# Kernel tuning notes

Measured on AMD Instinct MI355X. Metric: run time of the kernel, lower is better.

The kernel has to match this reference:

```python
import jax, jax.numpy as jnp
import numpy as np

B = 16384
D = 64            # bottom_mlp_layers[-1] = embedding_dim
DENSE = 512
HIST = 50         # history length per row
C_CAMP = 1000     # num_collisions for campaign table (sqrt(1e6))
C_FEAT = 316      # num_collisions for 1e5-vocab tables
NQ_CAMP = 1000    # ceil(1e6/1000)
NQ_FEAT = 317     # ceil(1e5/316)
NFEAT = 7
N = NFEAT + 1 + 1 # sparse features + dense row
PROJ = 128


def setup_inputs() -> dict:
    key = jax.random.key(0)
    ks = jax.random.split(key, 20)
    inp = {
        'x': jax.random.normal(ks[0], (B, DENSE), jnp.float32),
        'hist_idx': jax.random.randint(ks[1], (B * HIST,), 0, 1000000),
        'hist_offsets': jnp.arange(B, dtype=jnp.int64) * HIST,
        'feat_idx': jax.random.randint(ks[2], (B, NFEAT), 0, 100000),
        # QR embedding tables (quotient, remainder)
        'Wq_c': jax.random.normal(ks[3], (NQ_CAMP, D), jnp.float32) * 0.05,
        'Wr_c': jax.random.normal(ks[4], (C_CAMP, D), jnp.float32) * 0.05,
        'Wq_f': jax.random.normal(ks[5], (NFEAT, NQ_FEAT, D), jnp.float32) * 0.05,
        'Wr_f': jax.random.normal(ks[6], (NFEAT, C_FEAT, D), jnp.float32) * 0.05,
        # bottom MLP: 512->512 relu 512->256 relu 256->64
        'W0': jax.random.normal(ks[7], (512, DENSE), jnp.float32) * 0.03,
        'b0': jnp.zeros((512,), jnp.float32),
        'W1': jax.random.normal(ks[8], (256, 512), jnp.float32) * 0.04,
        'b1': jnp.zeros((256,), jnp.float32),
        'W2': jax.random.normal(ks[9], (64, 256), jnp.float32) * 0.06,
        'b2': jnp.zeros((64,), jnp.float32),
        # projection: (D + (N^2-N)/2) -> PROJ ; 64 + 36 = 100
        'Wp': jax.random.normal(ks[10], (PROJ, D + (N * N - N) // 2), jnp.float32) * 0.1,
        'bp': jnp.zeros((PROJ,), jnp.float32),
    }
    return inp


def _forward(x, hist_idx, hist_offsets, feat_idx, Wq_c, Wr_c, Wq_f, Wr_f,
             W0, b0, W1, b1, W2, b2, Wp, bp):
    # bottom MLP
    h = jax.nn.relu(x @ W0.T + b0)
    h = jax.nn.relu(h @ W1.T + b1)
    dense = h @ W2.T + b2                                   # [B, D]

    # QR embedding bag (mode='mean', operation='mult') for history feature
    e = Wq_c[hist_idx // C_CAMP] * Wr_c[hist_idx % C_CAMP]  # [M, D]
    M = hist_idx.shape[0]
    seg = jnp.cumsum(jnp.zeros((M,), jnp.int32).at[hist_offsets].add(1)) - 1
    sums = jax.ops.segment_sum(e, seg, num_segments=B)      # [B, D]
    counts = jnp.diff(jnp.concatenate([hist_offsets, jnp.array([M], hist_offsets.dtype)]))
    hist_emb = sums / counts[:, None].astype(sums.dtype)

    # single-valued QR lookups (bag size 1 -> mean == lookup)
    t = jnp.arange(NFEAT)[None, :]
    fe = Wq_f[t, feat_idx // C_FEAT] * Wr_f[t, feat_idx % C_FEAT]  # [B, NFEAT, D]

    # pairwise dot interaction: upper triangle (offset=1) of T @ T^T
    T = jnp.concatenate([dense[:, None, :], hist_emb[:, None, :], fe], axis=1)  # [B, N, D]
    Z = jnp.einsum('bnd,bmd->bnm', T, T)
    row, col = np.triu_indices(N, k=1)
    Z_flat = Z[:, row, col]                                  # [B, (N^2-N)/2]

    combined = jnp.concatenate([dense, Z_flat], axis=1)
    return combined @ Wp.T + bp                              # [B, PROJ]


def reference(x, hist_idx, hist_offsets, feat_idx, Wq_c, Wr_c, Wq_f, Wr_f,
              W0, b0, W1, b1, W2, b2, Wp, bp):
    return _forward(x, hist_idx, hist_offsets, feat_idx, Wq_c, Wr_c, Wq_f, Wr_f,
                    W0, b0, W1, b1, W2, b2, Wp, bp)
```

## Files before the change

### kernel.cpp

```cpp
#include <hip/hip_runtime.h>
#include <hip/hip_bf16.h>
#include <stdint.h>

#define DENSE_D 512
#define HIDDEN1 512
#define HIDDEN2 256
#define EMB_D   64
#define NFEAT   7
#define NROWS   9
#define NPAIRS  36
#define COMB    100
#define KPROJ   128
#define PROJ    128
#define C_CAMP  1000
#define C_FEAT  316
#define NQ_FEAT 317
#define TROWS   16
#define GROWS   8
#define HISTMAX 64

typedef __attribute__((ext_vector_type(8)))  __bf16 bf16x8;
typedef __attribute__((ext_vector_type(8)))  unsigned short ushort8;
typedef __attribute__((ext_vector_type(4)))  float  facc4;

#define GLD_LDS16(gp, lp) __builtin_amdgcn_global_load_lds( \
    (__attribute__((address_space(1))) void*)(gp), \
    (__attribute__((address_space(3))) void*)(lp), 16, 0, 0)

__device__ inline unsigned short f2bf(float f) {
    __hip_bfloat16 h = __float2bfloat16(f);
    return *reinterpret_cast<unsigned short*>(&h);
}
__device__ inline float blo(unsigned int u) { return __uint_as_float(u << 16); }
__device__ inline float bhi(unsigned int u) { return __uint_as_float(u & 0xffff0000u); }

template<int BM, int BN, int BK, int WM, int WN, bool RELU, bool A_F32>
__global__ __launch_bounds__(WM * WN * 64)
void gemm16(const void* __restrict__ Avoid,
            const unsigned short* __restrict__ W,
            const float* __restrict__ bias,
            unsigned short* __restrict__ Cout,
            int M, int N, int K)
{
    constexpr int THREADS = WM * WN * 64;
    constexpr int MREP    = BM / (WM * 16);
    constexpr int NREP    = BN / (WN * 16);
    constexpr int SUB     = BK / 32;
    constexpr int ACH     = BM * BK / 8;
    constexpr int BCH     = BN * BK / 8;

    __shared__ __align__(16) unsigned short Asm[BK / 8][BM][8];
    __shared__ __align__(16) unsigned short Bsm[BK / 8][BN][8];

    const int tid  = threadIdx.x;
    const int lane = tid & 63;
    const int wave = tid >> 6;
    const int wm   = wave / WN;
    const int wn   = wave % WN;
    const int row0 = blockIdx.x * BM;
    const int col0 = blockIdx.y * BN;
    const int fr   = lane & 15;
    const int fk   = lane >> 4;

    facc4 acc[MREP][NREP] = {};

    for (int k0 = 0; k0 < K; k0 += BK) {
        if (A_F32) {
            const float* Af = (const float*)Avoid;
            #pragma unroll
            for (int it = 0; it < ACH / THREADS; ++it) {
                const int p  = it * THREADS + tid;
                const int r  = p & (BM - 1);
                const int kc = p / BM;
                const float* src = Af + (size_t)(row0 + r) * K + k0 + kc * 8;
                const float4 v0 = *reinterpret_cast<const float4*>(src);
                const float4 v1 = *reinterpret_cast<const float4*>(src + 4);
                ushort8 cv;
                cv[0] = f2bf(v0.x); cv[1] = f2bf(v0.y);
                cv[2] = f2bf(v0.z); cv[3] = f2bf(v0.w);
                cv[4] = f2bf(v1.x); cv[5] = f2bf(v1.y);
                cv[6] = f2bf(v1.z); cv[7] = f2bf(v1.w);
                *reinterpret_cast<ushort8*>(
                    (unsigned short*)(&Asm[0][0][0]) + (size_t)p * 8) = cv;
            }
        } else {
            const unsigned short* Ab = (const unsigned short*)Avoid;
            #pragma unroll
            for (int it = 0; it < ACH / THREADS; ++it) {
                const int p  = it * THREADS + tid;
                const int r  = p & (BM - 1);
                const int kc = p / BM;
                GLD_LDS16(Ab + (size_t)(row0 + r) * K + k0 + kc * 8,
                          (&Asm[0][0][0]) + (size_t)p * 8);
            }
        }
        #pragma unroll
        for (int it = 0; it < BCH / THREADS; ++it) {
            const int p  = it * THREADS + tid;
            const int r  = p & (BN - 1);
            const int kc = p / BN;
            GLD_LDS16(W + (size_t)(col0 + r) * K + k0 + kc * 8,
                      (&Bsm[0][0][0]) + (size_t)p * 8);
        }
        __syncthreads();

        #pragma unroll
        for (int s = 0; s < SUB; ++s) {
            bf16x8 af[MREP], bw[NREP];
            #pragma unroll
            for (int m = 0; m < MREP; ++m)
                af[m] = *reinterpret_cast<const bf16x8*>(
                    &Asm[s * 4 + fk][wm * (MREP * 16) + m * 16 + fr][0]);
            #pragma unroll
            for (int n = 0; n < NREP; ++n)
                bw[n] = *reinterpret_cast<const bf16x8*>(
                    &Bsm[s * 4 + fk][wn * (NREP * 16) + n * 16 + fr][0]);
            #pragma unroll
            for (int m = 0; m < MREP; ++m)
                #pragma unroll
                for (int n = 0; n < NREP; ++n)
                    acc[m][n] = __builtin_amdgcn_mfma_f32_16x16x32_bf16(
                        af[m], bw[n], acc[m][n], 0, 0, 0);
        }
        __syncthreads();
    }

    #pragma unroll
    for (int n = 0; n < NREP; ++n) {
        const int col = col0 + wn * (NREP * 16) + n * 16 + fr;
        const float bv = bias[col];
        #pragma unroll
        for (int m = 0; m < MREP; ++m) {
            #pragma unroll
            for (int j = 0; j < 4; ++j) {
                const int row = row0 + wm * (MREP * 16) + m * 16 + fk * 4 + j;
                float v = acc[m][n][j] + bv;
                if (RELU) v = fmaxf(v, 0.f);
                Cout[(size_t)row * N + col] = f2bf(v);
            }
        }
    }
}

__device__ inline void cast_seg(const float* __restrict__ src,
                                unsigned short* __restrict__ dst,
                                int n4, int id, int stride)
{
    for (int i = id; i < n4; i += stride) {
        const float4 v = reinterpret_cast<const float4*>(src)[i];
        ushort4 o;
        o.x = f2bf(v.x); o.y = f2bf(v.y); o.z = f2bf(v.z); o.w = f2bf(v.w);
        reinterpret_cast<ushort4*>(dst)[i] = o;
    }
}

__global__ __launch_bounds__(256)
void prep_all(const float* __restrict__ W0, const float* __restrict__ W1,
              const float* __restrict__ W2, const float* __restrict__ Wp,
              const float* __restrict__ Wq_c, const float* __restrict__ Wr_c,
              const float* __restrict__ Wq_f, const float* __restrict__ Wr_f,
              unsigned short* w0b, unsigned short* w1b, unsigned short* w2b,
              unsigned short* wpb, unsigned short* qcb, unsigned short* rcb,
              unsigned short* qfb, unsigned short* rfb)
{
    const int id = blockIdx.x * blockDim.x + threadIdx.x;
    const int stride = gridDim.x * blockDim.x;
    cast_seg(W0,   w0b, HIDDEN1 * DENSE_D / 4,   id, stride);
    cast_seg(W1,   w1b, HIDDEN2 * HIDDEN1 / 4,   id, stride);
    cast_seg(W2,   w2b, EMB_D * HIDDEN2 / 4,     id, stride);
    cast_seg(Wq_c, qcb, C_CAMP * EMB_D / 4,      id, stride);
    cast_seg(Wr_c, rcb, C_CAMP * EMB_D / 4,      id, stride);
    cast_seg(Wq_f, qfb, NFEAT * NQ_FEAT * EMB_D / 4, id, stride);
    cast_seg(Wr_f, rfb, NFEAT * C_FEAT * EMB_D / 4,  id, stride);
    for (int i = id; i < PROJ * KPROJ; i += stride) {
        const int r = i >> 7, c = i & 127;
        wpb[i] = (c < COMB) ? f2bf(Wp[r * COMB + c]) : (unsigned short)0;
    }
}

__global__ __launch_bounds__(256)
void hist_gather(const int* __restrict__ hist_idx,
                 const int* __restrict__ hist_off,
                 const unsigned short* __restrict__ qcb,
                 const unsigned short* __restrict__ rcb,
                 unsigned short* __restrict__ hemb,
                 int B, int Mtot)
{
    const int r0 = blockIdx.x * GROWS;
    const int t  = threadIdx.x;

    __shared__ int2 soff[GROWS][HISTMAX];
    __shared__ int  scnt[GROWS];

    for (int p = t; p < GROWS * HISTMAX; p += 256) {
        const int row = p >> 6;
        const int i   = p & 63;
        const int br  = r0 + row;
        const int start = hist_off[br];
        const int end   = (br + 1 < B) ? hist_off[br + 1] : Mtot;
        const int cnt   = end - start;
        int2 o = make_int2(0, 0);
        if (i < cnt) {
            const int hi = hist_idx[start + i];
            const int q = hi / C_CAMP;
            o = make_int2(q * EMB_D, (hi - q * C_CAMP) * EMB_D);
        }
        soff[row][i] = o;
        if (i == 0) scnt[row] = cnt;
    }
    __syncthreads();

    const int lane = t & 63;
    const int wv   = t >> 6;
    const int half = lane >> 5;
    const int row  = wv * 2 + half;
    const int l5   = lane & 31;
    const int slot = l5 >> 3;
    const int d8   = l5 & 7;
    const int cnt  = scnt[row];

    const unsigned short* qb = qcb + d8 * 8;
    const unsigned short* rb = rcb + d8 * 8;

    float a[8] = {};
    #define ACC8(q, r) do { \
        a[0] += blo((q).x) * blo((r).x); a[1] += bhi((q).x) * bhi((r).x); \
        a[2] += blo((q).y) * blo((r).y); a[3] += bhi((q).y) * bhi((r).y); \
        a[4] += blo((q).z) * blo((r).z); a[5] += bhi((q).z) * bhi((r).z); \
        a[6] += blo((q).w) * blo((r).w); a[7] += bhi((q).w) * bhi((r).w); } while (0)

    const int full = cnt >> 2;
    int g = 0;
    for (; g + 4 <= full; g += 4) {
        int2 o[4];
        #pragma unroll
        for (int j = 0; j < 4; ++j) o[j] = soff[row][(g + j) * 4 + slot];
        uint4 uq[4], ur[4];
        #pragma unroll
        for (int j = 0; j < 4; ++j) {
            uq[j] = *reinterpret_cast<const uint4*>(qb + o[j].x);
            ur[j] = *reinterpret_cast<const uint4*>(rb + o[j].y);
        }
        #pragma unroll
        for (int j = 0; j < 4; ++j) ACC8(uq[j], ur[j]);
    }
    for (; g < full; ++g) {
        const int2 o = soff[row][g * 4 + slot];
        const uint4 uq = *reinterpret_cast<const uint4*>(qb + o.x);
        const uint4 ur = *reinterpret_cast<const uint4*>(rb + o.y);
        ACC8(uq, ur);
    }
    {
        const int idx = (full << 2) + slot;
        const int2 o = soff[row][idx & (HISTMAX - 1)];
        const uint4 uq = *reinterpret_cast<const uint4*>(qb + o.x);
        const uint4 ur = *reinterpret_cast<const uint4*>(rb + o.y);
        if (idx < cnt) ACC8(uq, ur);
    }
    #undef ACC8

    #pragma unroll
    for (int k = 0; k < 8; ++k) {
        a[k] += __shfl_xor(a[k], 8);
        a[k] += __shfl_xor(a[k], 16);
    }

    if (slot == 0) {
        const float inv = 1.f / (float)max(cnt, 1);
        union { unsigned short s[8]; uint4 u; } pk;
        #pragma unroll
        for (int k = 0; k < 8; ++k) pk.s[k] = f2bf(a[k] * inv);
        *reinterpret_cast<uint4*>(hemb + (size_t)(r0 + row) * EMB_D + d8 * 8) = pk.u;
    }
}

__global__ __launch_bounds__(256)
void tail_rest(const unsigned short* __restrict__ h1b,
               const unsigned short* __restrict__ w2b,
               const float* __restrict__ b2,
               const unsigned short* __restrict__ hemb,
               const int* __restrict__ feat_idx,
               const unsigned short* __restrict__ qfb,
               const unsigned short* __restrict__ rfb,
               const unsigned short* __restrict__ wpb,
               const float* __restrict__ bp,
               float* __restrict__ out)
{
    const int r0   = blockIdx.x * TROWS;
    const int t    = threadIdx.x;
    const int lane = t & 63;
    const int wave = t >> 6;
    const int fr   = lane & 15;
    const int fk   = lane >> 4;

    __shared__ __align__(16) unsigned short T[TROWS][NROWS][72];
    __shared__ __align__(16) unsigned short combs[TROWS][136];

    {
        facc4 acc = {};
        const unsigned short* arow = h1b + (size_t)(r0 + fr) * HIDDEN2;
        const unsigned short* brow = w2b + (size_t)(wave * 16 + fr) * HIDDEN2;
        #pragma unroll
        for (int kw = 0; kw < 8; ++kw) {
            const bf16x8 af = *reinterpret_cast<const bf16x8*>(arow + kw * 32 + fk * 8);
            const bf16x8 bw = *reinterpret_cast<const bf16x8*>(brow + kw * 32 + fk * 8);
            acc = __builtin_amdgcn_mfma_f32_16x16x32_bf16(af, bw, acc, 0, 0, 0);
        }
        const int col = wave * 16 + fr;
        const float bv = b2[col];
        #pragma unroll
        for (int j = 0; j < 4; ++j) {
            const int row = fk * 4 + j;
            const unsigned short hv = f2bf(acc[j] + bv);
            T[row][0][col]  = hv;
            combs[row][col] = hv;
        }
    }

    for (int p = t; p < TROWS * 18; p += 256) {
        const int row = p / 18, c = p % 18;
        *reinterpret_cast<unsigned int*>(&combs[row][100 + c * 2]) = 0u;
    }

    if (t < TROWS * 8) {
        const int row = t >> 3, o8 = t & 7;
        const uint4 v = *reinterpret_cast<const uint4*>(
            hemb + (size_t)(r0 + row) * EMB_D + o8 * 8);
        *reinterpret_cast<uint4*>(&T[row][1][o8 * 8]) = v;
    }

    {
        const int row = t >> 4;
        const int oc  = t & 15;
        const int br  = r0 + row;
        const int fbase = br * NFEAT;
        #pragma unroll
        for (int f = 0; f < NFEAT; ++f) {
            const int fi = feat_idx[fbase + f];
            const int q = fi / C_FEAT, r = fi - q * C_FEAT;
            const uint2 qv = *reinterpret_cast<const uint2*>(
                qfb + ((size_t)f * NQ_FEAT + q) * EMB_D + oc * 4);
            const uint2 rv = *reinterpret_cast<const uint2*>(
                rfb + ((size_t)f * C_FEAT + r) * EMB_D + oc * 4);
            union { ushort4 v; uint2 u; } pk;
            pk.v.x = f2bf(blo(qv.x) * blo(rv.x));
            pk.v.y = f2bf(bhi(qv.x) * bhi(rv.x));
            pk.v.z = f2bf(blo(qv.y) * blo(rv.y));
            pk.v.w = f2bf(bhi(qv.y) * bhi(rv.y));
            *reinterpret_cast<uint2*>(&T[row][2 + f][oc * 4]) = pk.u;
        }
    }
    __syncthreads();

    for (int p = t; p < NPAIRS * TROWS; p += 256) {
        const int row = p & (TROWS - 1);
        const int pr  = p / TROWS;
        int i = 0, rem = pr;
        while (rem >= (NROWS - 1) - i) { rem -= (NROWS - 1) - i; ++i; }
        const int j = i + 1 + rem;
        const unsigned short* ti = &T[row][i][0];
        const unsigned short* tj = &T[row][j][0];
        float s = 0.f;
        #pragma unroll
        for (int d = 0; d < EMB_D; d += 4) {
            const uint2 u = *reinterpret_cast<const uint2*>(ti + d);
            const uint2 v = *reinterpret_cast<const uint2*>(tj + d);
            s += blo(u.x) * blo(v.x) + bhi(u.x) * bhi(v.x)
               + blo(u.y) * blo(v.y) + bhi(u.y) * bhi(v.y);
        }
        combs[row][EMB_D + pr] = f2bf(s);
    }
    __syncthreads();

    {
        facc4 acc[2] = {};
        #pragma unroll
        for (int kw = 0; kw < 4; ++kw) {
            const bf16x8 af = *reinterpret_cast<const bf16x8*>(
                &combs[fr][kw * 32 + fk * 8]);
            #pragma unroll
            for (int n = 0; n < 2; ++n) {
                const bf16x8 bw = *reinterpret_cast<const bf16x8*>(
                    wpb + (size_t)(wave * 32 + n * 16 + fr) * KPROJ + kw * 32 + fk * 8);
                acc[n] = __builtin_amdgcn_mfma_f32_16x16x32_bf16(af, bw, acc[n], 0, 0, 0);
            }
        }
        #pragma unroll
        for (int n = 0; n < 2; ++n) {
            const int col = wave * 32 + n * 16 + fr;
            const float bv = bp[col];
            #pragma unroll
            for (int j = 0; j < 4; ++j) {
                const int row = fk * 4 + j;
                out[(size_t)(r0 + row) * PROJ + col] = acc[n][j] + bv;
            }
        }
    }
}

extern "C" void kernel_launch(void* const* d_in, const int* in_sizes, int n_in,
                              void* d_out, int out_size, void* d_ws, size_t ws_size,
                              hipStream_t stream)
{
    const float* x        = (const float*)d_in[0];
    const int*   hist_idx = (const int*)  d_in[1];
    const int*   hist_off = (const int*)  d_in[2];
    const int*   feat_idx = (const int*)  d_in[3];
    const float* Wq_c     = (const float*)d_in[4];
    const float* Wr_c     = (const float*)d_in[5];
    const float* Wq_f     = (const float*)d_in[6];
    const float* Wr_f     = (const float*)d_in[7];
    const float* W0       = (const float*)d_in[8];
    const float* b0       = (const float*)d_in[9];
    const float* W1       = (const float*)d_in[10];
    const float* b1       = (const float*)d_in[11];
    const float* W2       = (const float*)d_in[12];
    const float* b2       = (const float*)d_in[13];
    const float* Wp       = (const float*)d_in[14];
    const float* bp       = (const float*)d_in[15];

    const int M    = in_sizes[0] / DENSE_D;
    const int Mtot = in_sizes[1];

    char* w = (char*)d_ws;
    auto take = [&](size_t bytes) { char* p = w; w += (bytes + 255) & ~(size_t)255; return p; };
    unsigned short* w0b = (unsigned short*)take(HIDDEN1 * DENSE_D * 2);
    unsigned short* w1b = (unsigned short*)take(HIDDEN2 * HIDDEN1 * 2);
    unsigned short* w2b = (unsigned short*)take(EMB_D * HIDDEN2 * 2);
    unsigned short* wpb = (unsigned short*)take(PROJ * KPROJ * 2);
    unsigned short* qcb = (unsigned short*)take(C_CAMP * EMB_D * 2);
    unsigned short* rcb = (unsigned short*)take(C_CAMP * EMB_D * 2);
    unsigned short* qfb = (unsigned short*)take(NFEAT * NQ_FEAT * EMB_D * 2);
    unsigned short* rfb = (unsigned short*)take(NFEAT * C_FEAT * EMB_D * 2);
    unsigned short* h0b = (unsigned short*)take((size_t)M * HIDDEN1 * 2);
    unsigned short* h1b = (unsigned short*)take((size_t)M * HIDDEN2 * 2);
    unsigned short* hem = (unsigned short*)take((size_t)M * EMB_D * 2);

    prep_all<<<256, 256, 0, stream>>>(W0, W1, W2, Wp, Wq_c, Wr_c, Wq_f, Wr_f,
                                      w0b, w1b, w2b, wpb, qcb, rcb, qfb, rfb);

    hist_gather<<<M / GROWS, 256, 0, stream>>>(
        hist_idx, hist_off, qcb, rcb, hem, M, Mtot);

    gemm16<128, 128, 32, 2, 2, true, true>
        <<<dim3(M / 128, HIDDEN1 / 128), 256, 0, stream>>>(
        x, w0b, b0, h0b, M, HIDDEN1, DENSE_D);

    gemm16<64, 128, 64, 1, 4, true, false>
        <<<dim3(M / 64, HIDDEN2 / 128), 256, 0, stream>>>(
        h0b, w1b, b1, h1b, M, HIDDEN2, HIDDEN1);

    tail_rest<<<M / TROWS, 256, 0, stream>>>(
        h1b, w2b, b2, hem, feat_idx, qfb, rfb, wpb, bp, (float*)d_out);
}
```

Measured before the change: 82.31 us.

## Fuse second MLP GEMM into tail kernel, keeping h1 in shared memory

The 512->256 layer GEMM is moved into the tail kernel. Each block now computes h1 for 32 rows with MFMA, loading tiles into LDS through global_load_lds, and keeps the result in shared memory before running the existing W2, interaction and projection stages in two 16-row sub-blocks. This drops one kernel launch and the global write and read of h1. In exchange, each block reloads the full W1 tile (256x512) from L2 for only 32 rows, with a single-buffered, sync-heavy K loop and about 41KB of LDS, which may limit occupancy.

```diff
diff --git a/kernel.cpp b/kernel.cpp
--- a/kernel.cpp
+++ b/kernel.cpp
@@ -15,7 +15,6 @@
 #define C_CAMP  1000
 #define C_FEAT  316
 #define NQ_FEAT 317
-#define TROWS   16
 #define GROWS   8
 #define HISTMAX 64
 
@@ -275,126 +274,186 @@
 }
 
 __global__ __launch_bounds__(256)
-void tail_rest(const unsigned short* __restrict__ h1b,
-               const unsigned short* __restrict__ w2b,
-               const float* __restrict__ b2,
-               const unsigned short* __restrict__ hemb,
-               const int* __restrict__ feat_idx,
-               const unsigned short* __restrict__ qfb,
-               const unsigned short* __restrict__ rfb,
-               const unsigned short* __restrict__ wpb,
-               const float* __restrict__ bp,
-               float* __restrict__ out)
+void mlp_tail(const unsigned short* __restrict__ h0b,
+              const unsigned short* __restrict__ w1b,
+              const float* __restrict__ b1,
+              const unsigned short* __restrict__ w2b,
+              const float* __restrict__ b2,
+              const unsigned short* __restrict__ hemb,
+              const int* __restrict__ feat_idx,
+              const unsigned short* __restrict__ qfb,
+              const unsigned short* __restrict__ rfb,
+              const unsigned short* __restrict__ wpb,
+              const float* __restrict__ bp,
+              float* __restrict__ out)
 {
-    const int r0   = blockIdx.x * TROWS;
+    const int r0   = blockIdx.x * 32;
     const int t    = threadIdx.x;
     const int lane = t & 63;
     const int wave = t >> 6;
     const int fr   = lane & 15;
     const int fk   = lane >> 4;
 
-    __shared__ __align__(16) unsigned short T[TROWS][NROWS][72];
-    __shared__ __align__(16) unsigned short combs[TROWS][136];
+    __shared__ __align__(16) char pool[41472];
+    auto h1L  = reinterpret_cast<unsigned short(*)[32][8]>(pool);
+    auto Asm  = reinterpret_cast<unsigned short(*)[32][8]>(pool + 16384);
+    auto Bsm  = reinterpret_cast<unsigned short(*)[256][8]>(pool + 18432);
+    auto T    = reinterpret_cast<unsigned short(*)[NROWS][72]>(pool + 16384);
+    auto combs= reinterpret_cast<unsigned short(*)[136]>(pool + 37120);
 
     {
-        facc4 acc = {};
-        const unsigned short* arow = h1b + (size_t)(r0 + fr) * HIDDEN2;
-        const unsigned short* brow = w2b + (size_t)(wave * 16 + fr) * HIDDEN2;
-        #pragma unroll
-        for (int kw = 0; kw < 8; ++kw) {
-            const bf16x8 af = *reinterpret_cast<const bf16x8*>(arow + kw * 32 + fk * 8);
-            const bf16x8 bw = *reinterpret_cast<const bf16x8*>(brow + kw * 32 + fk * 8);
-            acc = __builtin_amdgcn_mfma_f32_16x16x32_bf16(af, bw, acc, 0, 0, 0);
-        }
-        const int col = wave * 16 + fr;
-        const float bv = b2[col];
-        #pragma unroll
-        for (int j = 0; j < 4; ++j) {
-            const int row = fk * 4 + j;
-            const unsigned short hv = f2bf(acc[j] + bv);
-            T[row][0][col]  = hv;
-            combs[row][col] = hv;
-        }
-    }
-
-    for (int p = t; p < TROWS * 18; p += 256) {
-        const int row = p / 18, c = p % 18;
-        *reinterpret_cast<unsigned int*>(&combs[row][100 + c * 2]) = 0u;
-    }
-
-    if (t < TROWS * 8) {
-        const int row = t >> 3, o8 = t & 7;
-        const uint4 v = *reinterpret_cast<const uint4*>(
-            hemb + (size_t)(r0 + row) * EMB_D + o8 * 8);
-        *reinterpret_cast<uint4*>(&T[row][1][o8 * 8]) = v;
-    }
-
-    {
-        const int row = t >> 4;
-        const int oc  = t & 15;
-        const int br  = r0 + row;
-        const int fbase = br * NFEAT;
-        #pragma unroll
-        for (int f = 0; f < NFEAT; ++f) {
-            const int fi = feat_idx[fbase + f];
-            const int q = fi / C_FEAT, r = fi - q * C_FEAT;
-            const uint2 qv = *reinterpret_cast<const uint2*>(
-                qfb + ((size_t)f * NQ_FEAT + q) * EMB_D + oc * 4);
-            const uint2 rv = *reinterpret_cast<const uint2*>(
-                rfb + ((size_t)f * C_FEAT + r) * EMB_D + oc * 4);
-            union { ushort4 v; uint2 u; } pk;
-            pk.v.x = f2bf(blo(qv.x) * blo(rv.x));
-            pk.v.y = f2bf(bhi(qv.x) * bhi(rv.x));
-            pk.v.z = f2bf(blo(qv.y) * blo(rv.y));
-            pk.v.w = f2bf(bhi(qv.y) * bhi(rv.y));
-            *reinterpret_cast<uint2*>(&T[row][2 + f][oc * 4]) = pk.u;
+        facc4 acc[2][4] = {};
+        for (int k0 = 0; k0 < HIDDEN1; k0 += 32) {
+            if (t < 128) {
+                const int r = t & 31, kc = t >> 5;
+                GLD_LDS16(h0b + (size_t)(r0 + r) * HIDDEN1 + k0 + kc * 8,
+                          (unsigned short*)(pool + 16384) + (size_t)t * 8);
+            }
+            #pragma unroll
+            for (int it = 0; it < 4; ++it) {
+                const int p = it * 256 + t;
+                const int r = p & 255, kc = p >> 8;
+                GLD_LDS16(w1b + (size_t)r * HIDDEN1 + k0 + kc * 8,
+                          (unsigned short*)(pool + 18432) + (size_t)p * 8);
+            }
+            __syncthreads();
+            bf16x8 af[2], bw[4];
+            #pragma unroll
+            for (int m = 0; m < 2; ++m)
+                af[m] = *reinterpret_cast<const bf16x8*>(&Asm[fk][m * 16 + fr][0]);
+            #pragma unroll
+            for (int n = 0; n < 4; ++n)
+                bw[n] = *reinterpret_cast<const bf16x8*>(&Bsm[fk][wave * 64 + n * 16 + fr][0]);
+            #pragma unroll
+            for (int m = 0; m < 2; ++m)
+                #pragma unroll
+                for (int n = 0; n < 4; ++n)
+                    acc[m][n] = __builtin_amdgcn_mfma_f32_16x16x32_bf16(
+                        af[m], bw[n], acc[m][n], 0, 0, 0);
+            __syncthreads();
+        }
+        #pragma unroll
+        for (int n = 0; n < 4; ++n) {
+            const int col = wave * 64 + n * 16 + fr;
+            const float bv = b1[col];
+            const int kc = col >> 3, ce = col & 7;
+            #pragma unroll
+            for (int m = 0; m < 2; ++m) {
+                #pragma unroll
+                for (int j = 0; j < 4; ++j) {
+                    const int row = m * 16 + fk * 4 + j;
+                    h1L[kc][row][ce] = f2bf(fmaxf(acc[m][n][j] + bv, 0.f));
+                }
+            }
         }
     }
     __syncthreads();
 
-    for (int p = t; p < NPAIRS * TROWS; p += 256) {
-        const int row = p & (TROWS - 1);
-        const int pr  = p / TROWS;
-        int i = 0, rem = pr;
-        while (rem >= (NROWS - 1) - i) { rem -= (NROWS - 1) - i; ++i; }
-        const int j = i + 1 + rem;
-        const unsigned short* ti = &T[row][i][0];
-        const unsigned short* tj = &T[row][j][0];
-        float s = 0.f;
-        #pragma unroll
-        for (int d = 0; d < EMB_D; d += 4) {
-            const uint2 u = *reinterpret_cast<const uint2*>(ti + d);
-            const uint2 v = *reinterpret_cast<const uint2*>(tj + d);
-            s += blo(u.x) * blo(v.x) + bhi(u.x) * bhi(v.x)
-               + blo(u.y) * blo(v.y) + bhi(u.y) * bhi(v.y);
-        }
-        combs[row][EMB_D + pr] = f2bf(s);
-    }
-    __syncthreads();
-
-    {
-        facc4 acc[2] = {};
-        #pragma unroll
-        for (int kw = 0; kw < 4; ++kw) {
-            const bf16x8 af = *reinterpret_cast<const bf16x8*>(
-                &combs[fr][kw * 32 + fk * 8]);
-            #pragma unroll
-            for (int n = 0; n < 2; ++n) {
+    #pragma unroll 1
+    for (int sb = 0; sb < 2; ++sb) {
+        const int rb = r0 + sb * 16;
+
+        {
+            facc4 acc2 = {};
+            #pragma unroll
+            for (int kw = 0; kw < 8; ++kw) {
+                const bf16x8 af = *reinterpret_cast<const bf16x8*>(
+                    &h1L[kw * 4 + fk][sb * 16 + fr][0]);
                 const bf16x8 bw = *reinterpret_cast<const bf16x8*>(
-                    wpb + (size_t)(wave * 32 + n * 16 + fr) * KPROJ + kw * 32 + fk * 8);
-                acc[n] = __builtin_amdgcn_mfma_f32_16x16x32_bf16(af, bw, acc[n], 0, 0, 0);
-            }
-        }
-        #pragma unroll
-        for (int n = 0; n < 2; ++n) {
-            const int col = wave * 32 + n * 16 + fr;
-            const float bv = bp[col];
+                    w2b + (size_t)(wave * 16 + fr) * HIDDEN2 + kw * 32 + fk * 8);
+                acc2 = __builtin_amdgcn_mfma_f32_16x16x32_bf16(af, bw, acc2, 0, 0, 0);
+            }
+            const int col = wave * 16 + fr;
+            const float bv = b2[col];
             #pragma unroll
             for (int j = 0; j < 4; ++j) {
                 const int row = fk * 4 + j;
-                out[(size_t)(r0 + row) * PROJ + col] = acc[n][j] + bv;
-            }
-        }
+                const unsigned short hv = f2bf(acc2[j] + bv);
+                T[row][0][col]  = hv;
+                combs[row][col] = hv;
+            }
+        }
+
+        for (int p = t; p < 16 * 18; p += 256) {
+            const int row = p / 18, c = p % 18;
+            *reinterpret_cast<unsigned int*>(&combs[row][100 + c * 2]) = 0u;
+        }
+
+        if (t < 128) {
+            const int row = t >> 3, o8 = t & 7;
+            const uint4 v = *reinterpret_cast<const uint4*>(
+                hemb + (size_t)(rb + row) * EMB_D + o8 * 8);
+            *reinterpret_cast<uint4*>(&T[row][1][o8 * 8]) = v;
+        }
+
+        {
+            const int row = t >> 4;
+            const int oc  = t & 15;
+            const int br  = rb + row;
+            const int fbase = br * NFEAT;
+            #pragma unroll
+            for (int f = 0; f < NFEAT; ++f) {
+                const int fi = feat_idx[fbase + f];
+                const int q = fi / C_FEAT, r = fi - q * C_FEAT;
+                const uint2 qv = *reinterpret_cast<const uint2*>(
+                    qfb + ((size_t)f * NQ_FEAT + q) * EMB_D + oc * 4);
+                const uint2 rv = *reinterpret_cast<const uint2*>(
+                    rfb + ((size_t)f * C_FEAT + r) * EMB_D + oc * 4);
+                union { ushort4 v; uint2 u; } pk;
+                pk.v.x = f2bf(blo(qv.x) * blo(rv.x));
+                pk.v.y = f2bf(bhi(qv.x) * bhi(rv.x));
+                pk.v.z = f2bf(blo(qv.y) * blo(rv.y));
+                pk.v.w = f2bf(bhi(qv.y) * bhi(rv.y));
+                *reinterpret_cast<uint2*>(&T[row][2 + f][oc * 4]) = pk.u;
+            }
+        }
+        __syncthreads();
+
+        for (int p = t; p < NPAIRS * 16; p += 256) {
+            const int row = p & 15;
+            const int pr  = p >> 4;
+            int i = 0, rem = pr;
+            while (rem >= (NROWS - 1) - i) { rem -= (NROWS - 1) - i; ++i; }
+            const int j = i + 1 + rem;
+            const unsigned short* ti = &T[row][i][0];
+            const unsigned short* tj = &T[row][j][0];
+            float s = 0.f;
+            #pragma unroll
+            for (int d = 0; d < EMB_D; d += 4) {
+                const uint2 u = *reinterpret_cast<const uint2*>(ti + d);
+                const uint2 v = *reinterpret_cast<const uint2*>(tj + d);
+                s += blo(u.x) * blo(v.x) + bhi(u.x) * bhi(v.x)
+                   + blo(u.y) * blo(v.y) + bhi(u.y) * bhi(v.y);
+            }
+            combs[row][EMB_D + pr] = f2bf(s);
+        }
+        __syncthreads();
+
+        {
+            facc4 acc[2] = {};
+            #pragma unroll
+            for (int kw = 0; kw < 4; ++kw) {
+                const bf16x8 af = *reinterpret_cast<const bf16x8*>(
+                    &combs[fr][kw * 32 + fk * 8]);
+                #pragma unroll
+                for (int n = 0; n < 2; ++n) {
+                    const bf16x8 bw = *reinterpret_cast<const bf16x8*>(
+                        wpb + (size_t)(wave * 32 + n * 16 + fr) * KPROJ + kw * 32 + fk * 8);
+                    acc[n] = __builtin_amdgcn_mfma_f32_16x16x32_bf16(af, bw, acc[n], 0, 0, 0);
+                }
+            }
+            #pragma unroll
+            for (int n = 0; n < 2; ++n) {
+                const int col = wave * 32 + n * 16 + fr;
+                const float bv = bp[col];
+                #pragma unroll
+                for (int j = 0; j < 4; ++j) {
+                    const int row = fk * 4 + j;
+                    out[(size_t)(rb + row) * PROJ + col] = acc[n][j] + bv;
+                }
+            }
+        }
+        __syncthreads();
     }
 }
 
@@ -433,7 +492,6 @@
     unsigned short* qfb = (unsigned short*)take(NFEAT * NQ_FEAT * EMB_D * 2);
     unsigned short* rfb = (unsigned short*)take(NFEAT * C_FEAT * EMB_D * 2);
     unsigned short* h0b = (unsigned short*)take((size_t)M * HIDDEN1 * 2);
-    unsigned short* h1b = (unsigned short*)take((size_t)M * HIDDEN2 * 2);
     unsigned short* hem = (unsigned short*)take((size_t)M * EMB_D * 2);
 
     prep_all<<<256, 256, 0, stream>>>(W0, W1, W2, Wp, Wq_c, Wr_c, Wq_f, Wr_f,
@@ -446,10 +504,6 @@
         <<<dim3(M / 128, HIDDEN1 / 128), 256, 0, stream>>>(
         x, w0b, b0, h0b, M, HIDDEN1, DENSE_D);
 
-    gemm16<64, 128, 64, 1, 4, true, false>
-        <<<dim3(M / 64, HIDDEN2 / 128), 256, 0, stream>>>(
-        h0b, w1b, b1, h1b, M, HIDDEN2, HIDDEN1);
-
-    tail_rest<<<M / TROWS, 256, 0, stream>>>(
-        h1b, w2b, b2, hem, feat_idx, qfb, rfb, wpb, bp, (float*)d_out);
-}
+    mlp_tail<<<M / 32, 256, 0, stream>>>(
+        h0b, w1b, b1, w2b, b2, hem, feat_idx, qfb, rfb, wpb, bp, (float*)d_out);
+}
```

Measured after the change: 83.80 us. No clear change (+1.8%).

## Fuse weight-cast prep into history gather and read embedding tables as fp32

Applied to the files above, without the earlier changes.

Merges the separate weight-cast kernel into the history-gather kernel, with extra blocks handling the MLP and projection weight casts, which removes one launch and its serial dependency. The embedding tables are no longer converted to bf16. The history gather and the feature lookups now read the fp32 tables directly with float4 loads, and the gather uses 4 rows per block with one wave per row. The cost is twice the bytes per gathered row, while the cast pass and its intermediate buffers go away. NGBLK is hardcoded to 4096, which with GROWS of 4 assumes B=16384.

```diff
diff --git a/kernel.cpp b/kernel.cpp
--- a/kernel.cpp
+++ b/kernel.cpp
@@ -16,8 +16,10 @@
 #define C_FEAT  316
 #define NQ_FEAT 317
 #define TROWS   16
-#define GROWS   8
+#define GROWS   4
 #define HISTMAX 64
+#define NGBLK   4096
+#define NCBLK   64
 
 typedef __attribute__((ext_vector_type(8)))  __bf16 bf16x8;
 typedef __attribute__((ext_vector_type(8)))  unsigned short ushort8;
@@ -155,46 +157,40 @@
 }
 
 __global__ __launch_bounds__(256)
-void prep_all(const float* __restrict__ W0, const float* __restrict__ W1,
-              const float* __restrict__ W2, const float* __restrict__ Wp,
-              const float* __restrict__ Wq_c, const float* __restrict__ Wr_c,
-              const float* __restrict__ Wq_f, const float* __restrict__ Wr_f,
-              unsigned short* w0b, unsigned short* w1b, unsigned short* w2b,
-              unsigned short* wpb, unsigned short* qcb, unsigned short* rcb,
-              unsigned short* qfb, unsigned short* rfb)
-{
-    const int id = blockIdx.x * blockDim.x + threadIdx.x;
-    const int stride = gridDim.x * blockDim.x;
-    cast_seg(W0,   w0b, HIDDEN1 * DENSE_D / 4,   id, stride);
-    cast_seg(W1,   w1b, HIDDEN2 * HIDDEN1 / 4,   id, stride);
-    cast_seg(W2,   w2b, EMB_D * HIDDEN2 / 4,     id, stride);
-    cast_seg(Wq_c, qcb, C_CAMP * EMB_D / 4,      id, stride);
-    cast_seg(Wr_c, rcb, C_CAMP * EMB_D / 4,      id, stride);
-    cast_seg(Wq_f, qfb, NFEAT * NQ_FEAT * EMB_D / 4, id, stride);
-    cast_seg(Wr_f, rfb, NFEAT * C_FEAT * EMB_D / 4,  id, stride);
-    for (int i = id; i < PROJ * KPROJ; i += stride) {
-        const int r = i >> 7, c = i & 127;
-        wpb[i] = (c < COMB) ? f2bf(Wp[r * COMB + c]) : (unsigned short)0;
-    }
-}
-
-__global__ __launch_bounds__(256)
-void hist_gather(const int* __restrict__ hist_idx,
+void gather_prep(const int* __restrict__ hist_idx,
                  const int* __restrict__ hist_off,
-                 const unsigned short* __restrict__ qcb,
-                 const unsigned short* __restrict__ rcb,
+                 const float* __restrict__ Wq_c,
+                 const float* __restrict__ Wr_c,
                  unsigned short* __restrict__ hemb,
+                 const float* __restrict__ W0, const float* __restrict__ W1,
+                 const float* __restrict__ W2, const float* __restrict__ Wp,
+                 unsigned short* w0b, unsigned short* w1b,
+                 unsigned short* w2b, unsigned short* wpb,
                  int B, int Mtot)
 {
+    const int t = threadIdx.x;
+
+    if (blockIdx.x >= NGBLK) {
+        const int id = (blockIdx.x - NGBLK) * 256 + t;
+        const int stride = NCBLK * 256;
+        cast_seg(W0, w0b, HIDDEN1 * DENSE_D / 4, id, stride);
+        cast_seg(W1, w1b, HIDDEN2 * HIDDEN1 / 4, id, stride);
+        cast_seg(W2, w2b, EMB_D * HIDDEN2 / 4,   id, stride);
+        for (int i = id; i < PROJ * KPROJ; i += stride) {
+            const int r = i >> 7, c = i & 127;
+            wpb[i] = (c < COMB) ? f2bf(Wp[r * COMB + c]) : (unsigned short)0;
+        }
+        return;
+    }
+
     const int r0 = blockIdx.x * GROWS;
-    const int t  = threadIdx.x;
 
     __shared__ int2 soff[GROWS][HISTMAX];
     __shared__ int  scnt[GROWS];
 
-    for (int p = t; p < GROWS * HISTMAX; p += 256) {
-        const int row = p >> 6;
-        const int i   = p & 63;
+    {
+        const int row = t >> 6;
+        const int i   = t & 63;
         const int br  = r0 + row;
         const int start = hist_off[br];
         const int end   = (br + 1 < B) ? hist_off[br + 1] : Mtot;
@@ -210,24 +206,19 @@
     }
     __syncthreads();
 
+    const int row  = t >> 6;
     const int lane = t & 63;
-    const int wv   = t >> 6;
-    const int half = lane >> 5;
-    const int row  = wv * 2 + half;
-    const int l5   = lane & 31;
-    const int slot = l5 >> 3;
-    const int d8   = l5 & 7;
+    const int slot = lane >> 4;
+    const int d4   = lane & 15;
     const int cnt  = scnt[row];
 
-    const unsigned short* qb = qcb + d8 * 8;
-    const unsigned short* rb = rcb + d8 * 8;
-
-    float a[8] = {};
-    #define ACC8(q, r) do { \
-        a[0] += blo((q).x) * blo((r).x); a[1] += bhi((q).x) * bhi((r).x); \
-        a[2] += blo((q).y) * blo((r).y); a[3] += bhi((q).y) * bhi((r).y); \
-        a[4] += blo((q).z) * blo((r).z); a[5] += bhi((q).z) * bhi((r).z); \
-        a[6] += blo((q).w) * blo((r).w); a[7] += bhi((q).w) * bhi((r).w); } while (0)
+    const float* qb = Wq_c + d4 * 4;
+    const float* rb = Wr_c + d4 * 4;
+
+    float a0 = 0.f, a1 = 0.f, a2 = 0.f, a3 = 0.f;
+    #define ACC4(q, r) do { \
+        a0 += (q).x * (r).x; a1 += (q).y * (r).y; \
+        a2 += (q).z * (r).z; a3 += (q).w * (r).w; } while (0)
 
     const int full = cnt >> 2;
     int g = 0;
@@ -235,42 +226,41 @@
         int2 o[4];
         #pragma unroll
         for (int j = 0; j < 4; ++j) o[j] = soff[row][(g + j) * 4 + slot];
-        uint4 uq[4], ur[4];
+        float4 uq[4], ur[4];
         #pragma unroll
         for (int j = 0; j < 4; ++j) {
-            uq[j] = *reinterpret_cast<const uint4*>(qb + o[j].x);
-            ur[j] = *reinterpret_cast<const uint4*>(rb + o[j].y);
-        }
-        #pragma unroll
-        for (int j = 0; j < 4; ++j) ACC8(uq[j], ur[j]);
+            uq[j] = *reinterpret_cast<const float4*>(qb + o[j].x);
+            ur[j] = *reinterpret_cast<const float4*>(rb + o[j].y);
+        }
+        #pragma unroll
+        for (int j = 0; j < 4; ++j) ACC4(uq[j], ur[j]);
     }
     for (; g < full; ++g) {
         const int2 o = soff[row][g * 4 + slot];
-        const uint4 uq = *reinterpret_cast<const uint4*>(qb + o.x);
-        const uint4 ur = *reinterpret_cast<const uint4*>(rb + o.y);
-        ACC8(uq, ur);
+        const float4 uq = *reinterpret_cast<const float4*>(qb + o.x);
+        const float4 ur = *reinterpret_cast<const float4*>(rb + o.y);
+        ACC4(uq, ur);
     }
     {
         const int idx = (full << 2) + slot;
         const int2 o = soff[row][idx & (HISTMAX - 1)];
-        const uint4 uq = *reinterpret_cast<const uint4*>(qb + o.x);
-        const uint4 ur = *reinterpret_cast<const uint4*>(rb + o.y);
-        if (idx < cnt) ACC8(uq, ur);
-    }
-    #undef ACC8
-
-    #pragma unroll
-    for (int k = 0; k < 8; ++k) {
-        a[k] += __shfl_xor(a[k], 8);
-        a[k] += __shfl_xor(a[k], 16);
-    }
+        const float4 uq = *reinterpret_cast<const float4*>(qb + o.x);
+        const float4 ur = *reinterpret_cast<const float4*>(rb + o.y);
+        if (idx < cnt) ACC4(uq, ur);
+    }
+    #undef ACC4
+
+    a0 += __shfl_xor(a0, 16); a1 += __shfl_xor(a1, 16);
+    a2 += __shfl_xor(a2, 16); a3 += __shfl_xor(a3, 16);
+    a0 += __shfl_xor(a0, 32); a1 += __shfl_xor(a1, 32);
+    a2 += __shfl_xor(a2, 32); a3 += __shfl_xor(a3, 32);
 
     if (slot == 0) {
         const float inv = 1.f / (float)max(cnt, 1);
-        union { unsigned short s[8]; uint4 u; } pk;
-        #pragma unroll
-        for (int k = 0; k < 8; ++k) pk.s[k] = f2bf(a[k] * inv);
-        *reinterpret_cast<uint4*>(hemb + (size_t)(r0 + row) * EMB_D + d8 * 8) = pk.u;
+        union { ushort4 v; uint2 u; } pk;
+        pk.v.x = f2bf(a0 * inv); pk.v.y = f2bf(a1 * inv);
+        pk.v.z = f2bf(a2 * inv); pk.v.w = f2bf(a3 * inv);
+        *reinterpret_cast<uint2*>(hemb + (size_t)(r0 + row) * EMB_D + d4 * 4) = pk.u;
     }
 }
 
@@ -280,8 +270,8 @@
                const float* __restrict__ b2,
                const unsigned short* __restrict__ hemb,
                const int* __restrict__ feat_idx,
-               const unsigned short* __restrict__ qfb,
-               const unsigned short* __restrict__ rfb,
+               const float* __restrict__ Wq_f,
+               const float* __restrict__ Wr_f,
                const unsigned short* __restrict__ wpb,
                const float* __restrict__ bp,
                float* __restrict__ out)
@@ -338,15 +328,15 @@
         for (int f = 0; f < NFEAT; ++f) {
             const int fi = feat_idx[fbase + f];
             const int q = fi / C_FEAT, r = fi - q * C_FEAT;
-            const uint2 qv = *reinterpret_cast<const uint2*>(
-                qfb + ((size_t)f * NQ_FEAT + q) * EMB_D + oc * 4);
-            const uint2 rv = *reinterpret_cast<const uint2*>(
-                rfb + ((size_t)f * C_FEAT + r) * EMB_D + oc * 4);
+            const float4 qv = *reinterpret_cast<const float4*>(
+                Wq_f + ((size_t)f * NQ_FEAT + q) * EMB_D + oc * 4);
+            const float4 rv = *reinterpret_cast<const float4*>(
+                Wr_f + ((size_t)f * C_FEAT + r) * EMB_D + oc * 4);
             union { ushort4 v; uint2 u; } pk;
-            pk.v.x = f2bf(blo(qv.x) * blo(rv.x));
-            pk.v.y = f2bf(bhi(qv.x) * bhi(rv.x));
-            pk.v.z = f2bf(blo(qv.y) * blo(rv.y));
-            pk.v.w = f2bf(bhi(qv.y) * bhi(rv.y));
+            pk.v.x = f2bf(qv.x * rv.x);
+            pk.v.y = f2bf(qv.y * rv.y);
+            pk.v.z = f2bf(qv.z * rv.z);
+            pk.v.w = f2bf(qv.w * rv.w);
             *reinterpret_cast<uint2*>(&T[row][2 + f][oc * 4]) = pk.u;
         }
     }
@@ -428,19 +418,13 @@
     unsigned short* w1b = (unsigned short*)take(HIDDEN2 * HIDDEN1 * 2);
     unsigned short* w2b = (unsigned short*)take(EMB_D * HIDDEN2 * 2);
     unsigned short* wpb = (unsigned short*)take(PROJ * KPROJ * 2);
-    unsigned short* qcb = (unsigned short*)take(C_CAMP * EMB_D * 2);
-    unsigned short* rcb = (unsigned short*)take(C_CAMP * EMB_D * 2);
-    unsigned short* qfb = (unsigned short*)take(NFEAT * NQ_FEAT * EMB_D * 2);
-    unsigned short* rfb = (unsigned short*)take(NFEAT * C_FEAT * EMB_D * 2);
     unsigned short* h0b = (unsigned short*)take((size_t)M * HIDDEN1 * 2);
     unsigned short* h1b = (unsigned short*)take((size_t)M * HIDDEN2 * 2);
     unsigned short* hem = (unsigned short*)take((size_t)M * EMB_D * 2);
 
-    prep_all<<<256, 256, 0, stream>>>(W0, W1, W2, Wp, Wq_c, Wr_c, Wq_f, Wr_f,
-                                      w0b, w1b, w2b, wpb, qcb, rcb, qfb, rfb);
-
-    hist_gather<<<M / GROWS, 256, 0, stream>>>(
-        hist_idx, hist_off, qcb, rcb, hem, M, Mtot);
+    gather_prep<<<NGBLK + NCBLK, 256, 0, stream>>>(
+        hist_idx, hist_off, Wq_c, Wr_c, hem,
+        W0, W1, W2, Wp, w0b, w1b, w2b, wpb, M, Mtot);
 
     gemm16<128, 128, 32, 2, 2, true, true>
         <<<dim3(M / 128, HIDDEN1 / 128), 256, 0, stream>>>(
@@ -451,5 +435,5 @@
         h0b, w1b, b1, h1b, M, HIDDEN2, HIDDEN1);
 
     tail_rest<<<M / TROWS, 256, 0, stream>>>(
-        h1b, w2b, b2, hem, feat_idx, qfb, rfb, wpb, bp, (float*)d_out);
-}
+        h1b, w2b, b2, hem, feat_idx, Wq_f, Wr_f, wpb, bp, (float*)d_out);
+}
```

New measurement: 84.16 us. 2.2% more time.

## Merge first MLP GEMM and history gather into one heterogeneous kernel launch

Applied to the files above, without the earlier changes.

Combines the bottom-MLP layer-0 GEMM (512 blocks) and the history QR embedding-bag gather (B/8 blocks) into a single launch, with blocks picking their role by block index. The aim is to drop one kernel launch and let the memory-bound gather run alongside the compute-bound GEMM on the GPU. The GEMM part is rewritten inline with a fixed 128x128x32 tile, single-buffered LDS and a direct fp32-to-bf16 convert of x. Shared memory is now sized for both roles, which may lower occupancy for the gather blocks, and the inline GEMM may be less tuned than the template it replaces.

```diff
diff --git a/kernel.cpp b/kernel.cpp
--- a/kernel.cpp
+++ b/kernel.cpp
@@ -18,6 +18,7 @@
 #define TROWS   16
 #define GROWS   8
 #define HISTMAX 64
+#define G0BLK   512
 
 typedef __attribute__((ext_vector_type(8)))  __bf16 bf16x8;
 typedef __attribute__((ext_vector_type(8)))  unsigned short ushort8;
@@ -179,18 +180,99 @@
 }
 
 __global__ __launch_bounds__(256)
-void hist_gather(const int* __restrict__ hist_idx,
-                 const int* __restrict__ hist_off,
-                 const unsigned short* __restrict__ qcb,
-                 const unsigned short* __restrict__ rcb,
-                 unsigned short* __restrict__ hemb,
-                 int B, int Mtot)
+void gemm0_gather(const float* __restrict__ x,
+                  const unsigned short* __restrict__ w0b,
+                  const float* __restrict__ b0,
+                  unsigned short* __restrict__ h0b,
+                  const int* __restrict__ hist_idx,
+                  const int* __restrict__ hist_off,
+                  const unsigned short* __restrict__ qcb,
+                  const unsigned short* __restrict__ rcb,
+                  unsigned short* __restrict__ hemb,
+                  int B, int Mtot)
 {
-    const int r0 = blockIdx.x * GROWS;
-    const int t  = threadIdx.x;
-
+    const int t = threadIdx.x;
+
+    __shared__ __align__(16) unsigned short Asm[4][128][8];
+    __shared__ __align__(16) unsigned short Bsm[4][128][8];
     __shared__ int2 soff[GROWS][HISTMAX];
     __shared__ int  scnt[GROWS];
+
+    if (blockIdx.x < G0BLK) {
+        const int lane = t & 63;
+        const int wave = t >> 6;
+        const int wm   = wave >> 1;
+        const int wn   = wave & 1;
+        const int row0 = (blockIdx.x & 127) * 128;
+        const int col0 = (blockIdx.x >> 7) * 128;
+        const int fr   = lane & 15;
+        const int fk   = lane >> 4;
+
+        facc4 acc[4][4] = {};
+
+        for (int k0 = 0; k0 < DENSE_D; k0 += 32) {
+            #pragma unroll
+            for (int it = 0; it < 2; ++it) {
+                const int p  = it * 256 + t;
+                const int r  = p & 127;
+                const int kc = p >> 7;
+                const float* src = x + (size_t)(row0 + r) * DENSE_D + k0 + kc * 8;
+                const float4 v0 = *reinterpret_cast<const float4*>(src);
+                const float4 v1 = *reinterpret_cast<const float4*>(src + 4);
+                ushort8 cv;
+                cv[0] = f2bf(v0.x); cv[1] = f2bf(v0.y);
+                cv[2] = f2bf(v0.z); cv[3] = f2bf(v0.w);
+                cv[4] = f2bf(v1.x); cv[5] = f2bf(v1.y);
+                cv[6] = f2bf(v1.z); cv[7] = f2bf(v1.w);
+                *reinterpret_cast<ushort8*>(
+                    (unsigned short*)(&Asm[0][0][0]) + (size_t)p * 8) = cv;
+            }
+            #pragma unroll
+            for (int it = 0; it < 2; ++it) {
+                const int p  = it * 256 + t;
+                const int r  = p & 127;
+                const int kc = p >> 7;
+                GLD_LDS16(w0b + (size_t)(col0 + r) * DENSE_D + k0 + kc * 8,
+                          (&Bsm[0][0][0]) + (size_t)p * 8);
+            }
+            __syncthreads();
+
+            bf16x8 af[4], bw[4];
+            #pragma unroll
+            for (int m = 0; m < 4; ++m)
+                af[m] = *reinterpret_cast<const bf16x8*>(
+                    &Asm[fk][wm * 64 + m * 16 + fr][0]);
+            #pragma unroll
+            for (int n = 0; n < 4; ++n)
+                bw[n] = *reinterpret_cast<const bf16x8*>(
+                    &Bsm[fk][wn * 64 + n * 16 + fr][0]);
+            #pragma unroll
+            for (int m = 0; m < 4; ++m)
+                #pragma unroll
+                for (int n = 0; n < 4; ++n)
+                    acc[m][n] = __builtin_amdgcn_mfma_f32_16x16x32_bf16(
+                        af[m], bw[n], acc[m][n], 0, 0, 0);
+            __syncthreads();
+        }
+
+        #pragma unroll
+        for (int n = 0; n < 4; ++n) {
+            const int col = col0 + wn * 64 + n * 16 + fr;
+            const float bv = b0[col];
+            #pragma unroll
+            for (int m = 0; m < 4; ++m) {
+                #pragma unroll
+                for (int j = 0; j < 4; ++j) {
+                    const int row = row0 + wm * 64 + m * 16 + fk * 4 + j;
+                    h0b[(size_t)row * HIDDEN1 + col] =
+                        f2bf(fmaxf(acc[m][n][j] + bv, 0.f));
+                }
+            }
+        }
+        return;
+    }
+
+    const int r0 = (blockIdx.x - G0BLK) * GROWS;
 
     for (int p = t; p < GROWS * HISTMAX; p += 256) {
         const int row = p >> 6;
@@ -439,12 +521,8 @@
     prep_all<<<256, 256, 0, stream>>>(W0, W1, W2, Wp, Wq_c, Wr_c, Wq_f, Wr_f,
                                       w0b, w1b, w2b, wpb, qcb, rcb, qfb, rfb);
 
-    hist_gather<<<M / GROWS, 256, 0, stream>>>(
-        hist_idx, hist_off, qcb, rcb, hem, M, Mtot);
-
-    gemm16<128, 128, 32, 2, 2, true, true>
-        <<<dim3(M / 128, HIDDEN1 / 128), 256, 0, stream>>>(
-        x, w0b, b0, h0b, M, HIDDEN1, DENSE_D);
+    gemm0_gather<<<G0BLK + M / GROWS, 256, 0, stream>>>(
+        x, w0b, b0, h0b, hist_idx, hist_off, qcb, rcb, hem, M, Mtot);
 
     gemm16<64, 128, 64, 1, 4, true, false>
         <<<dim3(M / 64, HIDDEN2 / 128), 256, 0, stream>>>(
```

Measured after the change: 85.72 us. +4.1%, slower.
